# Performance work log

Measured on AMD Instinct MI355X. Metric: run time of the kernel, lower is better.

The kernel has to match this reference:

```python
import jax, jax.numpy as jnp
import numpy as np

D_KEY, BANK_N = 128, 9720
BS, N = 1, 1620          # n = h*w = 30*54 (480p features, stride 16)
D_VAL, C, OBJ_N = 512, 512, 3


def setup_inputs() -> dict:
    key = jax.random.key(0)
    k1, k2, k3, k4, k5 = jax.random.split(key, 5)
    return {
        "keys_bank": jax.random.normal(k1, (D_KEY, BANK_N), dtype=jnp.float32),
        "q_in": jax.random.normal(k2, (BS, D_KEY, N), dtype=jnp.float32),
        "q_out": jax.random.normal(k3, (OBJ_N, C, N), dtype=jnp.float32),
        "values": jax.random.normal(k4, (OBJ_N, D_VAL, BANK_N), dtype=jnp.float32),
        "masks": jax.random.uniform(k5, (OBJ_N, 1, BANK_N), dtype=jnp.float32),
    }


def reference(keys_bank, q_in, q_out, values, masks):
    # p[b,k,n] = softmax_k( keys^T q_in / sqrt(d_key) )
    d_key = keys_bank.shape[0]
    scale = 1.0 / np.sqrt(d_key).astype(np.float32)
    p = jnp.einsum("dk,bdn->bkn", keys_bank, q_in) * scale
    p = jax.nn.softmax(p, axis=1)  # over bank dim

    # Batched over objects (original loops per object, sharing p)
    mem = jnp.einsum("ovk,bkn->obvn", values, p)       # (obj, bs, d_val, n)
    mask_mem = jnp.einsum("ouk,bkn->obun", masks, p)   # (obj, bs, 1, n)
    q_out_with_mask = q_out[:, None, :, :] * mask_mem  # (obj, bs, C, n)

    out = jnp.concatenate([mem, q_out_with_mask], axis=2)  # (obj, bs, d_val+C, n)
    return jnp.swapaxes(out, 0, 1)                          # (bs, obj, d_val+C, n)
```

## Files before the change

### kernel.cpp

```cpp
#include <hip/hip_runtime.h>
#include <hip/hip_bf16.h>

typedef unsigned short u16;
typedef unsigned char  u8;

#define D_KEY   128
#define BANK_N  9720
#define BANK_P  9728
#define N_TOK   1620
#define N_PAD   1664
#define OBJ_N   3
#define M_PAD   1664
#define LDCOL   1664
#define ONES_ROW 1539
#define QK_SCALE 0.08838834764831845f

typedef __bf16 bf16x8 __attribute__((ext_vector_type(8)));
typedef float  f32x4  __attribute__((ext_vector_type(4)));
typedef unsigned int u32x4 __attribute__((ext_vector_type(4)));
typedef int i32x8 __attribute__((ext_vector_type(8)));

__device__ __forceinline__ float bf2f(u16 u) {
  union { unsigned int i; float f; } v; v.i = ((unsigned int)u) << 16; return v.f;
}
__device__ __forceinline__ u16 f2bf(float f) {
  unsigned int x = __float_as_uint(f);
  unsigned int r = x + 0x7fffu + ((x >> 16) & 1u);
  return (u16)(r >> 16);
}
__device__ __forceinline__ unsigned pack_fp8x4(float a, float b, float c, float d) {
  unsigned v = __builtin_amdgcn_cvt_pk_fp8_f32(a, b, 0, false);
  v = __builtin_amdgcn_cvt_pk_fp8_f32(c, d, v, true);
  return v;
}
__device__ __forceinline__ u8 f2fp8(float a) {
  return (u8)(__builtin_amdgcn_cvt_pk_fp8_f32(a, 0.f, 0, false) & 0xff);
}

__device__ __forceinline__ void load_lds16(const void* g, void* l) {
  __builtin_amdgcn_global_load_lds(
      (const __attribute__((address_space(1))) void*)g,
      (__attribute__((address_space(3))) void*)l, 16, 0, 0);
}

__global__ void prep(const float* __restrict__ q, const float* __restrict__ keys,
                     const float* __restrict__ values, const float* __restrict__ masks,
                     u16* __restrict__ qT, u16* __restrict__ kT, u8* __restrict__ vm8) {
  __shared__ float t[64][65];
  int b = blockIdx.x;
  if (b < 832) {
    int idx = b * 256 + threadIdx.x;
    int n = idx >> 7, d = idx & 127;
    float v = (n < N_TOK) ? q[d * N_TOK + n] * QK_SCALE : 0.f;
    qT[idx] = f2bf(v);
    return;
  }
  if (b < 1136) {
    b -= 832;
    const int bk = (b % 152) * 64;
    const int bd = (b / 152) * 64;
    const int tx = threadIdx.x & 63;
    const int ty = threadIdx.x >> 6;
#pragma unroll
    for (int i = 0; i < 64; i += 4) {
      int d = bd + ty + i;
      int k = bk + tx;
      t[ty + i][tx] = (k < BANK_N) ? keys[(size_t)d * BANK_N + k] : 0.f;
    }
    __syncthreads();
#pragma unroll
    for (int i = 0; i < 64; i += 4) {
      int r = ty + i;
      kT[(size_t)(bk + r) * D_KEY + bd + tx] = f2bf(t[tx][r]);
    }
    return;
  }
  const int NV = BANK_P / 4;
  int idx = (b - 1136) * 256 + threadIdx.x;
  if (idx >= M_PAD * NV) return;
  int m = idx / NV;
  int k4 = (idx - m * NV) * 4;
  float4 v = make_float4(0.f, 0.f, 0.f, 0.f);
  if (m == ONES_ROW) {
    v.x = (k4     < BANK_N) ? 1.f : 0.f;
    v.y = (k4 + 1 < BANK_N) ? 1.f : 0.f;
    v.z = (k4 + 2 < BANK_N) ? 1.f : 0.f;
    v.w = (k4 + 3 < BANK_N) ? 1.f : 0.f;
  } else {
    const float* src = nullptr;
    if (m < 1536)          src = values + (size_t)m * BANK_N;
    else if (m < ONES_ROW) src = masks + (size_t)(m - 1536) * BANK_N;
    if (src) {
      if (k4 + 3 < BANK_N) v = *(const float4*)(src + k4);
      else {
        if (k4     < BANK_N) v.x = src[k4];
        if (k4 + 1 < BANK_N) v.y = src[k4 + 1];
        if (k4 + 2 < BANK_N) v.z = src[k4 + 2];
        if (k4 + 3 < BANK_N) v.w = src[k4 + 3];
      }
    }
  }
  *(unsigned*)(vm8 + (size_t)m * BANK_P + k4) = pack_fp8x4(v.x, v.y, v.z, v.w);
}

__global__ void gemm_qk(const u16* __restrict__ A, const u16* __restrict__ B,
                        u8* __restrict__ E8)
{
  __shared__ __align__(16) u16 sbuf[8192];
  u16* As = sbuf;
  u16* Bs = sbuf + 4096;

  const int tid  = threadIdx.x;
  const int wave = tid >> 6;
  const int lane = tid & 63;
  const int bn = blockIdx.x % 76, bm = blockIdx.x / 76;

  const u16* Abase = A + (size_t)bm * 128 * D_KEY;
  const u16* Bbase = B + (size_t)bn * 128 * D_KEY;

  const int r  = lane >> 2;
  const int c8 = (lane & 3) << 3;
  const int s0 = wave, s1 = wave + 4;

  f32x4 acc[4][4];
#pragma unroll
  for (int i = 0; i < 4; i++)
#pragma unroll
    for (int j = 0; j < 4; j++) acc[i][j] = (f32x4){0.f, 0.f, 0.f, 0.f};

  const int m_in = lane & 15;
  const int quad = lane >> 4;
  const int wm = (wave >> 1) * 64;
  const int wn = (wave & 1) * 64;

  for (int kt = 0; kt < D_KEY; kt += 32) {
    load_lds16(Abase + (size_t)(s0 * 16 + r) * D_KEY + kt + c8, &As[s0 * 512]);
    load_lds16(Abase + (size_t)(s1 * 16 + r) * D_KEY + kt + c8, &As[s1 * 512]);
    load_lds16(Bbase + (size_t)(s0 * 16 + r) * D_KEY + kt + c8, &Bs[s0 * 512]);
    load_lds16(Bbase + (size_t)(s1 * 16 + r) * D_KEY + kt + c8, &Bs[s1 * 512]);
    __syncthreads();

    bf16x8 af[4], bfr[4];
#pragma unroll
    for (int i = 0; i < 4; i++)
      af[i] = *(const bf16x8*)&As[(wm + i * 16 + m_in) * 32 + quad * 8];
#pragma unroll
    for (int j = 0; j < 4; j++)
      bfr[j] = *(const bf16x8*)&Bs[(wn + j * 16 + m_in) * 32 + quad * 8];
#pragma unroll
    for (int i = 0; i < 4; i++)
#pragma unroll
      for (int j = 0; j < 4; j++)
        acc[i][j] = __builtin_amdgcn_mfma_f32_16x16x32_bf16(af[i], bfr[j], acc[i][j], 0, 0, 0);
    __syncthreads();
  }

  u8* sb8 = (u8*)sbuf;
#pragma unroll
  for (int i = 0; i < 4; i++)
#pragma unroll
    for (int j = 0; j < 4; j++)
#pragma unroll
      for (int t = 0; t < 4; t++) {
        int row_l = wm + i * 16 + quad * 4 + t;
        int col_l = wn + j * 16 + m_in;
        bool valid = (bn * 128 + col_l) < BANK_N;
        sb8[(row_l << 7) + col_l] = valid ? f2fp8(__expf(acc[i][j][t])) : (u8)0;
      }
  __syncthreads();

  for (int chunk = tid; chunk < 1024; chunk += 256) {
    int row = chunk >> 3;
    int cu  = (chunk & 7) << 4;
    u32x4 v = *(const u32x4*)&sb8[(row << 7) + cu];
    *(u32x4*)&E8[(size_t)(bm * 128 + row) * BANK_P + bn * 128 + cu] = v;
  }
}

__global__ __launch_bounds__(256, 3)
void gemm_pv(const u8* __restrict__ A, const u8* __restrict__ B,
             u16* __restrict__ memC, int kChunk, size_t cPartStride)
{
  __shared__ __align__(16) u16 sbuf[16384];
  u8* As8 = (u8*)sbuf;
  u8* Bs8 = (u8*)sbuf + 16384;

  const int tid  = threadIdx.x;
  const int wave = tid >> 6;
  const int lane = tid & 63;

  int b = blockIdx.x;
  int bz = b / 169;
  int rr = b - bz * 169;
  int gid = rr / 52;
  int rem = rr - gid * 52;
  int width = (gid < 3) ? 4 : 1;
  int bm = rem / width;
  int bn = gid * 4 + (rem - bm * width);

  const int kbeg = bz * kChunk;
  const int kend = kbeg + kChunk;

  const u8* Abase = A + (size_t)bm * 128 * BANK_P;
  const u8* Bbase = B + (size_t)bn * 128 * BANK_P;

  const int srow  = lane >> 1;
  const int shalf = (((lane & 1) ^ ((lane >> 3) & 1)) << 4);

  f32x4 acc[4][4];
#pragma unroll
  for (int i = 0; i < 4; i++)
#pragma unroll
    for (int j = 0; j < 4; j++) acc[i][j] = (f32x4){0.f, 0.f, 0.f, 0.f};

  const int m_in = lane & 15;
  const int quad = lane >> 4;
  const int wm = (wave >> 1) * 64;
  const int wn = (wave & 1) * 64;
  const int fxor = ((m_in >> 2) & 1) << 4;

  const size_t arow_off = (size_t)(wave * 32 + srow) * BANK_P;

  for (int kt = kbeg; kt < kend; kt += 128) {
#pragma unroll
    for (int s = 0; s < 4; s++)
      load_lds16(Abase + arow_off + kt + s * 32 + shalf, As8 + s * 4096 + wave * 1024);
#pragma unroll
    for (int s = 0; s < 4; s++)
      load_lds16(Bbase + arow_off + kt + s * 32 + shalf, Bs8 + s * 4096 + wave * 1024);
    __syncthreads();

    i32x8 a8[4];
#pragma unroll
    for (int i = 0; i < 4; i++) {
      const u8* p = As8 + quad * 4096 + (wm + i * 16 + m_in) * 32;
      u32x4 lo = *(const u32x4*)(p + fxor);
      u32x4 hi = *(const u32x4*)(p + (fxor ^ 16));
      a8[i] = (i32x8){(int)lo[0], (int)lo[1], (int)lo[2], (int)lo[3],
                      (int)hi[0], (int)hi[1], (int)hi[2], (int)hi[3]};
    }
#pragma unroll
    for (int j = 0; j < 4; j++) {
      const u8* p = Bs8 + quad * 4096 + (wn + j * 16 + m_in) * 32;
      u32x4 lo = *(const u32x4*)(p + fxor);
      u32x4 hi = *(const u32x4*)(p + (fxor ^ 16));
      i32x8 b8 = (i32x8){(int)lo[0], (int)lo[1], (int)lo[2], (int)lo[3],
                         (int)hi[0], (int)hi[1], (int)hi[2], (int)hi[3]};
#pragma unroll
      for (int i = 0; i < 4; i++)
        acc[i][j] = __builtin_amdgcn_mfma_scale_f32_16x16x128_f8f6f4(
            a8[i], b8, acc[i][j], 0, 0,
            0, 0x7f7f7f7f, 0, 0x7f7f7f7f);
    }
    __syncthreads();
  }

  u16* Cg = memC + (size_t)bz * cPartStride;
#pragma unroll
  for (int h = 0; h < 2; h++) {
    __syncthreads();
    if ((wave >> 1) == h) {
#pragma unroll
      for (int i = 0; i < 4; i++)
#pragma unroll
        for (int j = 0; j < 4; j++)
#pragma unroll
          for (int t = 0; t < 4; t++) {
            int row_l = i * 16 + quad * 4 + t;
            int col_l = wn + j * 16 + m_in;
            sbuf[(row_l << 7) + col_l] = f2bf(acc[i][j][t]);
          }
    }
    __syncthreads();
    for (int chunk = tid; chunk < 1024; chunk += 256) {
      int row = chunk >> 4;
      int cu  = (chunk & 15) << 3;
      u32x4 v = *(const u32x4*)&sbuf[(row << 7) + cu];
      __builtin_nontemporal_store(
          v, (u32x4*)&Cg[(size_t)(bm * 128 + h * 64 + row) * LDCOL + bn * 128 + cu]);
    }
  }
}

__global__ void epilogue(const u16* __restrict__ memC, const float* __restrict__ q_out,
                         float* __restrict__ out, int nParts) {
  const int NV = N_TOK / 4;
  int idx = blockIdx.x * 256 + threadIdx.x;
  if (idx >= OBJ_N * 1024 * NV) return;
  int n4 = (idx % NV) * 4;
  int t = idx / NV;
  int c = t & 1023;
  int o = t >> 10;
  const size_t ps = (size_t)M_PAD * LDCOL;

  const u16* lbase = memC + (size_t)ONES_ROW * LDCOL + n4;
  float4 l = make_float4(0.f, 0.f, 0.f, 0.f);
  for (int z = 0; z < nParts; z++) {
    ushort4 v = *(const ushort4*)(lbase + z * ps);
    l.x += bf2f(v.x); l.y += bf2f(v.y); l.z += bf2f(v.z); l.w += bf2f(v.w);
  }

  size_t rowoff = (c < 512) ? (size_t)(o * 512 + c) * LDCOL
                            : (size_t)(1536 + o) * LDCOL;
  const u16* base = memC + rowoff + n4;
  float4 s = make_float4(0.f, 0.f, 0.f, 0.f);
  for (int z = 0; z < nParts; z++) {
    ushort4 v = *(const ushort4*)(base + z * ps);
    s.x += bf2f(v.x); s.y += bf2f(v.y); s.z += bf2f(v.z); s.w += bf2f(v.w);
  }
  float4 rv;
  float ix = 1.f / l.x, iy = 1.f / l.y, iz = 1.f / l.z, iw = 1.f / l.w;
  if (c < 512) {
    rv.x = s.x * ix; rv.y = s.y * iy; rv.z = s.z * iz; rv.w = s.w * iw;
  } else {
    float4 q = *(const float4*)(q_out + (size_t)(o * 512 + (c - 512)) * N_TOK + n4);
    rv.x = q.x * s.x * ix; rv.y = q.y * s.y * iy;
    rv.z = q.z * s.z * iz; rv.w = q.w * s.w * iw;
  }
  *(float4*)(out + (size_t)(o * 1024 + c) * N_TOK + n4) = rv;
}

extern "C" void kernel_launch(void* const* d_in, const int* in_sizes, int n_in,
                              void* d_out, int out_size, void* d_ws, size_t ws_size,
                              hipStream_t stream) {
  const float* keys   = (const float*)d_in[0];
  const float* q_in   = (const float*)d_in[1];
  const float* q_out  = (const float*)d_in[2];
  const float* values = (const float*)d_in[3];
  const float* masks  = (const float*)d_in[4];
  float* out = (float*)d_out;

  char* ws = (char*)d_ws;
  size_t off = 0;
  auto alloc = [&](size_t bytes) -> void* {
    void* p = ws + off; off += (bytes + 255) & ~(size_t)255; return p;
  };
  u16* qT  = (u16*)alloc((size_t)N_PAD * D_KEY * 2);
  u16* kT  = (u16*)alloc((size_t)BANK_P * D_KEY * 2);
  u8*  vm8 = (u8*)alloc((size_t)M_PAD * BANK_P);
  u8*  E8  = (u8*)alloc((size_t)N_PAD * BANK_P);

  int nParts = 4;
  while (nParts > 1 && off + (size_t)nParts * M_PAD * LDCOL * 2 > ws_size) nParts >>= 1;
  u16* memC = (u16*)alloc((size_t)nParts * M_PAD * LDCOL * 2);

  const int vmBlocks = (M_PAD * (BANK_P / 4) + 255) / 256;
  prep<<<1136 + vmBlocks, 256, 0, stream>>>(q_in, keys, values, masks, qT, kT, vm8);

  gemm_qk<<<988, 256, 0, stream>>>(qT, kT, E8);

  int kChunk = BANK_P / nParts;
  gemm_pv<<<dim3(169 * nParts), 256, 0, stream>>>(vm8, E8, memC, kChunk, (size_t)M_PAD * LDCOL);

  epilogue<<<(OBJ_N * 1024 * (N_TOK / 4) + 255) / 256, 256, 0, stream>>>(
      memC, q_out, out, nParts);
}
```

Baseline: 192.2 us.

## Fuse value FP8 conversion into QK GEMM launch and use 8-way uneven split-K

The fp32-to-fp8 conversion of values and masks moves out of the prep kernel and into extra blocks of the gemm_qk launch. It now runs alongside the QK GEMM tiles instead of delaying them, and prep shrinks to only the q and key transposes. The PV GEMM split-K count rises from 4 to 8, using uneven chunk lengths (1280 and 1152) that tile BANK_P exactly, to fill more CUs. The cost is a larger partial-sum buffer and more reduction work in the epilogue.

```diff
diff --git a/kernel.cpp b/kernel.cpp
--- a/kernel.cpp
+++ b/kernel.cpp
@@ -44,8 +44,7 @@
 }
 
 __global__ void prep(const float* __restrict__ q, const float* __restrict__ keys,
-                     const float* __restrict__ values, const float* __restrict__ masks,
-                     u16* __restrict__ qT, u16* __restrict__ kT, u8* __restrict__ vm8) {
+                     u16* __restrict__ qT, u16* __restrict__ kT) {
   __shared__ float t[64][65];
   int b = blockIdx.x;
   if (b < 832) {
@@ -55,65 +54,70 @@
     qT[idx] = f2bf(v);
     return;
   }
-  if (b < 1136) {
-    b -= 832;
-    const int bk = (b % 152) * 64;
-    const int bd = (b / 152) * 64;
-    const int tx = threadIdx.x & 63;
-    const int ty = threadIdx.x >> 6;
-#pragma unroll
-    for (int i = 0; i < 64; i += 4) {
-      int d = bd + ty + i;
-      int k = bk + tx;
-      t[ty + i][tx] = (k < BANK_N) ? keys[(size_t)d * BANK_N + k] : 0.f;
-    }
-    __syncthreads();
-#pragma unroll
-    for (int i = 0; i < 64; i += 4) {
-      int r = ty + i;
-      kT[(size_t)(bk + r) * D_KEY + bd + tx] = f2bf(t[tx][r]);
-    }
-    return;
-  }
-  const int NV = BANK_P / 4;
-  int idx = (b - 1136) * 256 + threadIdx.x;
-  if (idx >= M_PAD * NV) return;
-  int m = idx / NV;
-  int k4 = (idx - m * NV) * 4;
-  float4 v = make_float4(0.f, 0.f, 0.f, 0.f);
-  if (m == ONES_ROW) {
-    v.x = (k4     < BANK_N) ? 1.f : 0.f;
-    v.y = (k4 + 1 < BANK_N) ? 1.f : 0.f;
-    v.z = (k4 + 2 < BANK_N) ? 1.f : 0.f;
-    v.w = (k4 + 3 < BANK_N) ? 1.f : 0.f;
-  } else {
-    const float* src = nullptr;
-    if (m < 1536)          src = values + (size_t)m * BANK_N;
-    else if (m < ONES_ROW) src = masks + (size_t)(m - 1536) * BANK_N;
-    if (src) {
-      if (k4 + 3 < BANK_N) v = *(const float4*)(src + k4);
-      else {
-        if (k4     < BANK_N) v.x = src[k4];
-        if (k4 + 1 < BANK_N) v.y = src[k4 + 1];
-        if (k4 + 2 < BANK_N) v.z = src[k4 + 2];
-        if (k4 + 3 < BANK_N) v.w = src[k4 + 3];
-      }
-    }
-  }
-  *(unsigned*)(vm8 + (size_t)m * BANK_P + k4) = pack_fp8x4(v.x, v.y, v.z, v.w);
+  b -= 832;
+  const int bk = (b % 152) * 64;
+  const int bd = (b / 152) * 64;
+  const int tx = threadIdx.x & 63;
+  const int ty = threadIdx.x >> 6;
+#pragma unroll
+  for (int i = 0; i < 64; i += 4) {
+    int d = bd + ty + i;
+    int k = bk + tx;
+    t[ty + i][tx] = (k < BANK_N) ? keys[(size_t)d * BANK_N + k] : 0.f;
+  }
+  __syncthreads();
+#pragma unroll
+  for (int i = 0; i < 64; i += 4) {
+    int r = ty + i;
+    kT[(size_t)(bk + r) * D_KEY + bd + tx] = f2bf(t[tx][r]);
+  }
 }
 
 __global__ void gemm_qk(const u16* __restrict__ A, const u16* __restrict__ B,
-                        u8* __restrict__ E8)
+                        u8* __restrict__ E8,
+                        const float* __restrict__ values, const float* __restrict__ masks,
+                        u8* __restrict__ vm8)
 {
   __shared__ __align__(16) u16 sbuf[8192];
+
+  int blk = blockIdx.x;
+  const int tid = threadIdx.x;
+
+  if (blk >= 988) {
+    const int NV = BANK_P / 4;
+    int idx = (blk - 988) * 256 + tid;
+    if (idx >= M_PAD * NV) return;
+    int m = idx / NV;
+    int k4 = (idx - m * NV) * 4;
+    float4 v = make_float4(0.f, 0.f, 0.f, 0.f);
+    if (m == ONES_ROW) {
+      v.x = (k4     < BANK_N) ? 1.f : 0.f;
+      v.y = (k4 + 1 < BANK_N) ? 1.f : 0.f;
+      v.z = (k4 + 2 < BANK_N) ? 1.f : 0.f;
+      v.w = (k4 + 3 < BANK_N) ? 1.f : 0.f;
+    } else {
+      const float* src = nullptr;
+      if (m < 1536)          src = values + (size_t)m * BANK_N;
+      else if (m < ONES_ROW) src = masks + (size_t)(m - 1536) * BANK_N;
+      if (src) {
+        if (k4 + 3 < BANK_N) v = *(const float4*)(src + k4);
+        else {
+          if (k4     < BANK_N) v.x = src[k4];
+          if (k4 + 1 < BANK_N) v.y = src[k4 + 1];
+          if (k4 + 2 < BANK_N) v.z = src[k4 + 2];
+          if (k4 + 3 < BANK_N) v.w = src[k4 + 3];
+        }
+      }
+    }
+    *(unsigned*)(vm8 + (size_t)m * BANK_P + k4) = pack_fp8x4(v.x, v.y, v.z, v.w);
+    return;
+  }
+
   u16* As = sbuf;
   u16* Bs = sbuf + 4096;
-
-  const int tid  = threadIdx.x;
   const int wave = tid >> 6;
   const int lane = tid & 63;
-  const int bn = blockIdx.x % 76, bm = blockIdx.x / 76;
+  const int bn = blk % 76, bm = blk / 76;
 
   const u16* Abase = A + (size_t)bm * 128 * D_KEY;
   const u16* Bbase = B + (size_t)bn * 128 * D_KEY;
@@ -179,7 +183,7 @@
 
 __global__ __launch_bounds__(256, 3)
 void gemm_pv(const u8* __restrict__ A, const u8* __restrict__ B,
-             u16* __restrict__ memC, int kChunk, size_t cPartStride)
+             u16* __restrict__ memC, int nParts, size_t cPartStride)
 {
   __shared__ __align__(16) u16 sbuf[16384];
   u8* As8 = (u8*)sbuf;
@@ -198,8 +202,15 @@
   int bm = rem / width;
   int bn = gid * 4 + (rem - bm * width);
 
-  const int kbeg = bz * kChunk;
-  const int kend = kbeg + kChunk;
+  int kbeg, klen;
+  if (nParts == 8) {
+    if (bz < 4) { kbeg = bz * 1280; klen = 1280; }
+    else        { kbeg = 5120 + (bz - 4) * 1152; klen = 1152; }
+  } else {
+    klen = BANK_P / nParts;
+    kbeg = bz * klen;
+  }
+  const int kend = kbeg + klen;
 
   const u8* Abase = A + (size_t)bm * 128 * BANK_P;
   const u8* Bbase = B + (size_t)bn * 128 * BANK_P;
@@ -340,17 +351,16 @@
   u8*  vm8 = (u8*)alloc((size_t)M_PAD * BANK_P);
   u8*  E8  = (u8*)alloc((size_t)N_PAD * BANK_P);
 
-  int nParts = 4;
+  int nParts = 8;
   while (nParts > 1 && off + (size_t)nParts * M_PAD * LDCOL * 2 > ws_size) nParts >>= 1;
   u16* memC = (u16*)alloc((size_t)nParts * M_PAD * LDCOL * 2);
 
+  prep<<<1136, 256, 0, stream>>>(q_in, keys, qT, kT);
+
   const int vmBlocks = (M_PAD * (BANK_P / 4) + 255) / 256;
-  prep<<<1136 + vmBlocks, 256, 0, stream>>>(q_in, keys, values, masks, qT, kT, vm8);
-
-  gemm_qk<<<988, 256, 0, stream>>>(qT, kT, E8);
-
-  int kChunk = BANK_P / nParts;
-  gemm_pv<<<dim3(169 * nParts), 256, 0, stream>>>(vm8, E8, memC, kChunk, (size_t)M_PAD * LDCOL);
+  gemm_qk<<<988 + vmBlocks, 256, 0, stream>>>(qT, kT, E8, values, masks, vm8);
+
+  gemm_pv<<<dim3(169 * nParts), 256, 0, stream>>>(vm8, E8, memC, nParts, (size_t)M_PAD * LDCOL);
 
   epilogue<<<(OBJ_N * 1024 * (N_TOK / 4) + 255) / 256, 256, 0, stream>>>(
       memC, q_out, out, nParts);
```

New measurement: 208.2 us. 8.3% more time.
